# Performance work log

Hardware: AMD Instinct MI355X
Metric: run time of the kernel (lower is better)

Reference implementation:

```python
import jax, jax.numpy as jnp
import numpy as np

NUM_HEADS = 16
EPS = 1e-6


def setup_inputs() -> dict:
    key = jax.random.key(0)
    k1, k2, k3 = jax.random.split(key, 3)
    B, S, D = 4, 4096, 1024
    x = jax.random.normal(k1, (B, S, D), dtype=jnp.float32)
    # weights scaled like nn.Linear init (~1/sqrt(fan_in))
    Wqkv = jax.random.normal(k2, (D, 3 * D), dtype=jnp.float32) / np.sqrt(D)
    Wo = jax.random.normal(k3, (D, D), dtype=jnp.float32) / np.sqrt(D)
    return {"x": x, "Wqkv": Wqkv, "Wo": Wo}


def reference(x, Wqkv, Wo):
    B, S, D = x.shape
    H = NUM_HEADS
    hd = D // H
    qkv = x @ Wqkv                                   # [B,S,3D]
    qkv = qkv.reshape(B, S, 3, H, hd).transpose(2, 0, 3, 1, 4)
    Q, K, V = qkv[0], qkv[1], qkv[2]                 # [B,H,S,hd]
    # feature map: elu(x) + 1 (positive)
    Q = jax.nn.elu(Q) + 1.0
    K = jax.nn.elu(K) + 1.0
    # O(N d^2): KV state then Q contraction
    KV = jnp.einsum('bhnd,bhnv->bhdv', K, V)         # [B,H,hd,hd]
    out = jnp.einsum('bhnd,bhdv->bhnv', Q, KV)       # [B,H,S,hd]
    K_sum = K.sum(axis=2)                            # [B,H,hd]
    normalizer = jnp.einsum('bhnd,bhd->bhn', Q, K_sum)[..., None]  # [B,H,S,1]
    out = out / (normalizer + EPS)
    out = out.transpose(0, 2, 1, 3).reshape(B, S, D)
    return out @ Wo
```

## Files before the change

### kernel.cpp

```cpp
#include <hip/hip_runtime.h>

using u16 = unsigned short;
typedef __attribute__((ext_vector_type(8))) short short8;
typedef __attribute__((ext_vector_type(4))) float f32x4;

__device__ __forceinline__ u16 f2bf(float f) {
  unsigned int u = __float_as_uint(f);
  u = (u + 0x7FFFu + ((u >> 16) & 1u)) >> 16;
  return (u16)u;
}
__device__ __forceinline__ float bf2f(u16 v) {
  return __uint_as_float(((unsigned int)v) << 16);
}

__device__ __forceinline__ void gload16(const void* g, void* l) {
  __builtin_amdgcn_global_load_lds((const __attribute__((address_space(1))) void*)g,
                                   (__attribute__((address_space(3))) void*)l, 16, 0, 0);
}

#define B_ 4
#define S_ 4096
#define D_ 1024
#define H_ 16
#define HD_ 64
#define M_ (B_*S_)
#define N1_ (3*D_)
#define NSPLIT_ 4

#define OFF_XB    0ull
#define OFF_WQKVT (OFF_XB    + (size_t)M_*D_*2)
#define OFF_WOT   (OFF_WQKVT + (size_t)N1_*D_*2)
#define OFF_QBUF  (OFF_WOT   + (size_t)D_*D_*2)
#define OFF_KT    (OFF_QBUF  + (size_t)M_*D_*2)
#define OFF_VT    (OFF_KT    + (size_t)M_*D_*2)
#define OFF_KV    (OFF_VT    + (size_t)M_*D_*2)
#define OFF_KSUM  (OFF_KV    + (size_t)NSPLIT_*64*4096*4)
#define WS_NEEDED (OFF_KSUM  + (size_t)NSPLIT_*64*64*4)
#define OFF_WT    OFF_KT
#define OFF_KSG   (OFF_KT + (size_t)8*1024*1024)

__global__ __launch_bounds__(256) void prep_kernel(const float* __restrict__ x, u16* __restrict__ xb,
                                                   const float* __restrict__ Wqkv, u16* __restrict__ wqkvt,
                                                   const float* __restrict__ Wo, u16* __restrict__ wot)
{
  __shared__ float tile[32][33];
  int bid = blockIdx.x, tid = threadIdx.x;
  if (bid < 16384) {
    int i = bid * 256 + tid;
    float4 v = ((const float4*)x)[i];
    uint2 o;
    o.x = (unsigned)f2bf(v.x) | ((unsigned)f2bf(v.y) << 16);
    o.y = (unsigned)f2bf(v.z) | ((unsigned)f2bf(v.w) << 16);
    ((uint2*)xb)[i] = o;
    return;
  }
  const float* in; u16* out; int R, C, cb, rb;
  if (bid < 19456) {
    int t = bid - 16384;  in = Wqkv; out = wqkvt; R = D_; C = N1_;
    cb = t % 96; rb = t / 96;
  } else {
    int t = bid - 19456;  in = Wo; out = wot; R = D_; C = D_;
    cb = t % 32; rb = t / 32;
  }
  int tx = tid & 31, ty = tid >> 5;
  int c0 = cb * 32, r0 = rb * 32;
#pragma unroll
  for (int i = 0; i < 4; i++)
    tile[ty + i*8][tx] = in[(size_t)(r0 + ty + i*8) * C + c0 + tx];
  __syncthreads();
#pragma unroll
  for (int i = 0; i < 4; i++)
    out[(size_t)(c0 + ty + i*8) * R + r0 + tx] = f2bf(tile[tx][ty + i*8]);
}

template<int MODE>
__global__ __launch_bounds__(512, 2) void gemm256(
    const u16* __restrict__ A, const u16* __restrict__ Bt,
    float* __restrict__ Cf, u16* __restrict__ qout,
    u16* __restrict__ Kt, u16* __restrict__ Vt,
    int M, int N, int K)
{
  __shared__ __align__(16) char smem[131072];
  int tid = threadIdx.x;
  int w = tid >> 6, lane = tid & 63;
  int quad = lane >> 4, l16 = lane & 15;
  int wm = w >> 2, wn = w & 3;

  int nwg = gridDim.x * gridDim.y;
  int flat = blockIdx.y * gridDim.x + blockIdx.x;
  int wg = (flat & 7) * (nwg >> 3) + (flat >> 3);
  int bx = wg % gridDim.x, by = wg / gridDim.x;
  int bm = by * 256, bn = bx * 256;

  const u16* Bp;
  if constexpr (MODE == 2) Bp = Bt + ((size_t)(bm >> 12) << 20);
  else                     Bp = Bt;

  int prl = lane >> 3;
  int c4  = (lane & 7) ^ prl;
  int r0  = ((w << 3) + prl) * 2 + (c4 >> 2);
  int koff = (c4 & 3) * 8;
  const u16* gA0 = A  + (size_t)(bm + r0) * K + koff;
  const u16* gB0 = Bp + (size_t)(bn + r0) * K + koff;
  size_t rowskip = (size_t)128 * K;
  char* smemc = smem;
  int ldsAw = w * 1024;
  int ldsBw = 65536 + w * 1024;

  int ph = (((l16 & 1) << 2) | quad) ^ ((l16 >> 1) & 7);
  int baseA = wm * 8192 + (l16 >> 1) * 128 + ph * 16;
  int baseB = 65536 + wn * 4096 + (l16 >> 1) * 128 + ph * 16;

  f32x4 acc[8][4];
#pragma unroll
  for (int i = 0; i < 8; i++)
#pragma unroll
    for (int j = 0; j < 4; j++) acc[i][j] = (f32x4)0.0f;

  int nt = K >> 5;

#define STG(tt, slot) {                                                   \
    const u16* a0_ = gA0 + (tt) * 32;                                     \
    const u16* b0_ = gB0 + (tt) * 32;                                     \
    gload16(a0_,           smemc + (slot)*16384 + ldsAw);                 \
    gload16(a0_ + rowskip, smemc + (slot)*16384 + 8192 + ldsAw);          \
    gload16(b0_,           smemc + (slot)*16384 + ldsBw);                 \
    gload16(b0_ + rowskip, smemc + (slot)*16384 + 8192 + ldsBw);          \
  }

#define COMPUTE(slot) {                                                              \
    const char* sb = smemc + (slot) * 16384;                                         \
    short8 bfr[4], af[8];                                                            \
    _Pragma("unroll")                                                                \
    for (int nj = 0; nj < 4; nj++) bfr[nj] = *(const short8*)(sb + baseB + nj*1024); \
    _Pragma("unroll")                                                                \
    for (int mi = 0; mi < 8; mi++) af[mi] = *(const short8*)(sb + baseA + mi*1024);  \
    __builtin_amdgcn_s_setprio(1);                                                   \
    _Pragma("unroll")                                                                \
    for (int mi = 0; mi < 8; mi++)                                                   \
      _Pragma("unroll")                                                              \
      for (int nj = 0; nj < 4; nj++)                                                 \
        acc[mi][nj] = __builtin_amdgcn_mfma_f32_16x16x32_bf16(af[mi], bfr[nj],       \
                                                              acc[mi][nj], 0, 0, 0); \
    __builtin_amdgcn_s_setprio(0);                                                   \
  }

#define WAITBAR(n) {                                                      \
    asm volatile("s_waitcnt vmcnt(" #n ")" ::: "memory");                 \
    __builtin_amdgcn_s_barrier();                                         \
    asm volatile("" ::: "memory");                                        \
  }

  STG(0, 0); STG(1, 1); STG(2, 2);
  WAITBAR(8)

  for (int tb = 0; tb < nt - 4; tb += 4) {
#pragma unroll
    for (int i = 0; i < 4; ++i) {
      int t = tb + i;
      STG(t + 3, ((i + 3) & 3));
      COMPUTE(i)
      WAITBAR(8)
    }
  }

  STG(nt - 1, 3);
  COMPUTE(0)
  WAITBAR(8)
  COMPUTE(1)
  WAITBAR(4)
  COMPUTE(2)
  WAITBAR(0)
  COMPUTE(3)

#undef STG
#undef COMPUTE
#undef WAITBAR

  int colbase = bn + wn * 64;
  if constexpr (MODE != 1) {
#pragma unroll
    for (int mi = 0; mi < 8; mi++) {
      int row0 = bm + wm * 128 + mi * 16 + quad * 4;
#pragma unroll
      for (int nj = 0; nj < 4; nj++) {
        int col = colbase + nj * 16 + l16;
#pragma unroll
        for (int r = 0; r < 4; r++)
          Cf[(size_t)(row0 + r) * N + col] = acc[mi][nj][r];
      }
    }
  } else {
    int cls = colbase >> 10;
    if (cls == 0) {
#pragma unroll
      for (int mi = 0; mi < 8; mi++) {
        int row0 = bm + wm * 128 + mi * 16 + quad * 4;
#pragma unroll
        for (int nj = 0; nj < 4; nj++) {
          int col = colbase + nj * 16 + l16;
#pragma unroll
          for (int r = 0; r < 4; r++) {
            float v = acc[mi][nj][r];
            v = (v > 0.0f) ? (v + 1.0f) : __expf(v);
            qout[(size_t)(row0 + r) * D_ + col] = f2bf(v);
          }
        }
      }
    } else {
      int b = bm >> 12;
      int h = (colbase & 1023) >> 6;
      u16* dst = (cls == 1 ? Kt : Vt) + (size_t)((b * 16 + h) * 64) * 4096;
      int sb0 = (bm & 4095) + wm * 128;
      bool doElu = (cls == 1);
#pragma unroll
      for (int mi = 0; mi < 8; mi++) {
        int s = sb0 + mi * 16 + quad * 4;
#pragma unroll
        for (int nj = 0; nj < 4; nj++) {
          int d = nj * 16 + l16;
          float v0 = acc[mi][nj][0], v1 = acc[mi][nj][1], v2 = acc[mi][nj][2], v3 = acc[mi][nj][3];
          if (doElu) {
            v0 = (v0 > 0.0f) ? (v0 + 1.0f) : __expf(v0);
            v1 = (v1 > 0.0f) ? (v1 + 1.0f) : __expf(v1);
            v2 = (v2 > 0.0f) ? (v2 + 1.0f) : __expf(v2);
            v3 = (v3 > 0.0f) ? (v3 + 1.0f) : __expf(v3);
          }
          uint2 o;
          o.x = (unsigned)f2bf(v0) | ((unsigned)f2bf(v1) << 16);
          o.y = (unsigned)f2bf(v2) | ((unsigned)f2bf(v3) << 16);
          *(uint2*)(dst + (size_t)d * 4096 + s) = o;
        }
      }
    }
  }
}

__global__ __launch_bounds__(256) void kv_kernel(const u16* __restrict__ Kt,
                                                 const u16* __restrict__ Vt,
                                                 float* __restrict__ KVp,
                                                 float* __restrict__ Ksp)
{
  __shared__ float red[4096];
  __shared__ float redS[64];
  int tid = threadIdx.x;
  int bh = blockIdx.x;
  int ssplit = blockIdx.y;
  int wave = tid >> 6, lane = tid & 63, quad = lane >> 4, l16 = lane & 15;
  int sbase = ssplit * (S_ / NSPLIT_) + wave * (S_ / NSPLIT_ / 4);
  const u16* Kb = Kt + (size_t)bh * 64 * 4096;
  const u16* Vb = Vt + (size_t)bh * 64 * 4096;
  short8 ones;
#pragma unroll
  for (int e = 0; e < 8; ++e) ones[e] = (short)0x3F80;

  for (int i = tid; i < 4096; i += 256) red[i] = 0.0f;
  if (tid < 64) redS[tid] = 0.0f;

  f32x4 acc[4][4], accs[4];
#pragma unroll
  for (int i = 0; i < 4; i++) {
    accs[i] = (f32x4)0.0f;
#pragma unroll
    for (int j = 0; j < 4; j++) acc[i][j] = (f32x4)0.0f;
  }

  for (int kk = 0; kk < S_ / NSPLIT_ / 4 / 32; ++kk) {
    int s = sbase + kk * 32 + quad * 8;
    short8 af[4], bfr[4];
#pragma unroll
    for (int i = 0; i < 4; i++) {
      af[i]  = *(const short8*)(Kb + (size_t)(i*16 + l16) * 4096 + s);
      bfr[i] = *(const short8*)(Vb + (size_t)(i*16 + l16) * 4096 + s);
    }
#pragma unroll
    for (int i = 0; i < 4; i++) {
#pragma unroll
      for (int j = 0; j < 4; j++)
        acc[i][j] = __builtin_amdgcn_mfma_f32_16x16x32_bf16(af[i], bfr[j], acc[i][j], 0, 0, 0);
      accs[i] = __builtin_amdgcn_mfma_f32_16x16x32_bf16(af[i], ones, accs[i], 0, 0, 0);
    }
  }
  __syncthreads();
#pragma unroll
  for (int i = 0; i < 4; i++) {
    int d0 = i*16 + quad*4;
#pragma unroll
    for (int j = 0; j < 4; j++)
#pragma unroll
      for (int r = 0; r < 4; r++)
        atomicAdd(&red[(d0 + r) * 64 + j*16 + l16], acc[i][j][r]);
    if (l16 == 0)
#pragma unroll
      for (int r = 0; r < 4; r++)
        atomicAdd(&redS[d0 + r], accs[i][r]);
  }
  __syncthreads();
  float* dst = KVp + ((size_t)ssplit * 64 + bh) * 4096;
  for (int i = tid; i < 4096; i += 256) dst[i] = red[i];
  if (tid < 64) Ksp[((size_t)ssplit * 64 + bh) * 64 + tid] = redS[tid];
}

__global__ __launch_bounds__(256) void kvw_kernel(const float* __restrict__ KVp,
                                                  const float* __restrict__ Ksp,
                                                  const u16* __restrict__ wot,
                                                  u16* __restrict__ wt,
                                                  float* __restrict__ ksum)
{
  __shared__ u16 kvlds[4096];
  int tid = threadIdx.x;
  int ct = blockIdx.x;
  int bh = blockIdx.y;
  int b = bh >> 4, h = bh & 15;
  const float* kvsrc = KVp + (size_t)bh * 4096;
  for (int i = tid; i < 4096; i += 256) {
    float s = kvsrc[i] + kvsrc[i + 64*4096] + kvsrc[i + 2*64*4096] + kvsrc[i + 3*64*4096];
    kvlds[i] = f2bf(s);
  }
  if (ct == 0 && tid < 64) {
    const float* ks = Ksp + (size_t)bh * 64;
    ksum[bh * 64 + tid] = ks[tid] + ks[tid + 64*64] + ks[tid + 2*64*64] + ks[tid + 3*64*64];
  }
  __syncthreads();
  int w = tid >> 6, lane = tid & 63, quad = lane >> 4, l16 = lane & 15;

  short8 bfr[2][4];
#pragma unroll
  for (int ks = 0; ks < 2; ++ks)
#pragma unroll
    for (int nj = 0; nj < 4; ++nj)
      bfr[ks][nj] = *(const short8*)(&kvlds[(nj*16 + l16) * 64 + ks*32 + quad*8]);

  f32x4 acc[2][4];
#pragma unroll
  for (int i = 0; i < 2; i++)
#pragma unroll
    for (int j = 0; j < 4; j++) acc[i][j] = (f32x4)0.0f;

  int c0 = ct * 128 + w * 32;
#pragma unroll
  for (int ks = 0; ks < 2; ++ks) {
#pragma unroll
    for (int mi = 0; mi < 2; ++mi) {
      short8 af = *(const short8*)(wot + (size_t)(c0 + mi*16 + l16) * 1024 + h*64 + ks*32 + quad*8);
#pragma unroll
      for (int nj = 0; nj < 4; ++nj)
        acc[mi][nj] = __builtin_amdgcn_mfma_f32_16x16x32_bf16(af, bfr[ks][nj], acc[mi][nj], 0, 0, 0);
    }
  }
  u16* dst = wt + ((size_t)b << 20);
#pragma unroll
  for (int mi = 0; mi < 2; ++mi) {
    int c = c0 + mi*16 + quad*4;
#pragma unroll
    for (int nj = 0; nj < 4; ++nj) {
      int hd = h*64 + nj*16 + l16;
#pragma unroll
      for (int r = 0; r < 4; ++r)
        dst[(size_t)(c + r) * 1024 + hd] = f2bf(acc[mi][nj][r]);
    }
  }
}

__global__ __launch_bounds__(256) void qscale_kernel(u16* __restrict__ qbuf,
                                                     const float* __restrict__ ksum)
{
  __shared__ float ks[1024];
  int tid = threadIdx.x;
  int blk = blockIdx.x;
  int b = blk >> 10;
  for (int i = tid; i < 1024; i += 256) ks[i] = ksum[b * 1024 + i];
  __syncthreads();
  int wv = tid >> 6, ln = tid & 63;
  int s = blk * 4 + wv;
  u16* row = qbuf + (size_t)s * 1024 + ln * 16;
  short8 qa = *(const short8*)row;
  short8 qb = *(const short8*)(row + 8);
  int h4 = (ln >> 2) * 64 + (ln & 3) * 16;
  float p = 0.0f;
#pragma unroll
  for (int j = 0; j < 8; ++j) p += bf2f((u16)qa[j]) * ks[h4 + j];
#pragma unroll
  for (int j = 0; j < 8; ++j) p += bf2f((u16)qb[j]) * ks[h4 + 8 + j];
  p += __shfl_xor(p, 1);
  p += __shfl_xor(p, 2);
  float inv = 1.0f / (p + 1e-6f);
  short8 oa, ob;
#pragma unroll
  for (int j = 0; j < 8; ++j) {
    oa[j] = (short)f2bf(bf2f((u16)qa[j]) * inv);
    ob[j] = (short)f2bf(bf2f((u16)qb[j]) * inv);
  }
  *(short8*)row = oa;
  *(short8*)(row + 8) = ob;
}

extern "C" void kernel_launch(void* const* d_in, const int* in_sizes, int n_in,
                              void* d_out, int out_size, void* d_ws, size_t ws_size,
                              hipStream_t stream) {
  const float* x    = (const float*)d_in[0];
  const float* Wqkv = (const float*)d_in[1];
  const float* Wo   = (const float*)d_in[2];
  float* out = (float*)d_out;
  char* ws = (char*)d_ws;
  if (ws_size < WS_NEEDED) return;

  u16*   xb    = (u16*)  (ws + OFF_XB);
  u16*   wqkvt = (u16*)  (ws + OFF_WQKVT);
  u16*   wot   = (u16*)  (ws + OFF_WOT);
  u16*   qbuf  = (u16*)  (ws + OFF_QBUF);
  u16*   kt    = (u16*)  (ws + OFF_KT);
  u16*   vt    = (u16*)  (ws + OFF_VT);
  float* kvp   = (float*)(ws + OFF_KV);
  float* ksp   = (float*)(ws + OFF_KSUM);
  u16*   wt    = (u16*)  (ws + OFF_WT);
  float* ksg   = (float*)(ws + OFF_KSG);

  prep_kernel<<<20480, 256, 0, stream>>>(x, xb, Wqkv, wqkvt, Wo, wot);
  gemm256<1><<<dim3(N1_/256, M_/256), 512, 0, stream>>>(xb, wqkvt, nullptr, qbuf, kt, vt,
                                                        M_, N1_, D_);
  kv_kernel<<<dim3(64, NSPLIT_), 256, 0, stream>>>(kt, vt, kvp, ksp);
  kvw_kernel<<<dim3(8, 64), 256, 0, stream>>>(kvp, ksp, wot, wt, ksg);
  qscale_kernel<<<4096, 256, 0, stream>>>(qbuf, ksg);
  gemm256<2><<<dim3(D_/256, M_/256), 512, 0, stream>>>(qbuf, wt, out, nullptr, nullptr, nullptr,
                                                       M_, D_, D_);
}
```

Measured before the change: 337.8 us.

## Fuse K/V projection with per-tile KV outer-product reduction in GEMM epilogue

Splits the QKV projection into a Q-only GEMM and a K/V GEMM whose tiles pair matching K and V head columns. The K/V tile's epilogue stages the elu-transformed K and V in shared memory and computes partial K^T·V and K-sum per 256-row block with MFMA. This removes the global round trip of transposed K/V buffers and the separate kv_kernel. A new kvsum kernel reduces the 16 partials per batch-head. The cost is an extra epilogue in the GEMM, more partial-sum traffic, and two GEMM launches instead of one.

```diff
diff --git a/kernel.cpp b/kernel.cpp
--- a/kernel.cpp
+++ b/kernel.cpp
@@ -25,7 +25,6 @@
 #define HD_ 64
 #define M_ (B_*S_)
 #define N1_ (3*D_)
-#define NSPLIT_ 4
 
 #define OFF_XB    0ull
 #define OFF_WQKVT (OFF_XB    + (size_t)M_*D_*2)
@@ -34,10 +33,13 @@
 #define OFF_KT    (OFF_QBUF  + (size_t)M_*D_*2)
 #define OFF_VT    (OFF_KT    + (size_t)M_*D_*2)
 #define OFF_KV    (OFF_VT    + (size_t)M_*D_*2)
-#define OFF_KSUM  (OFF_KV    + (size_t)NSPLIT_*64*4096*4)
-#define WS_NEEDED (OFF_KSUM  + (size_t)NSPLIT_*64*64*4)
+#define OFF_KSUM  (OFF_KV    + (size_t)4*64*4096*4)
+#define WS_NEEDED (OFF_KSUM  + (size_t)4*64*64*4)
 #define OFF_WT    OFF_KT
-#define OFF_KSG   (OFF_KT + (size_t)8*1024*1024)
+#define OFF_KVS   (OFF_KT + ((size_t)8<<20))
+#define OFF_KSG   (OFF_KT + ((size_t)9<<20))
+#define OFF_KVPP  OFF_VT
+#define OFF_KSPP  (OFF_VT + ((size_t)16<<20))
 
 __global__ __launch_bounds__(256) void prep_kernel(const float* __restrict__ x, u16* __restrict__ xb,
                                                    const float* __restrict__ Wqkv, u16* __restrict__ wqkvt,
@@ -77,7 +79,7 @@
 __global__ __launch_bounds__(512, 2) void gemm256(
     const u16* __restrict__ A, const u16* __restrict__ Bt,
     float* __restrict__ Cf, u16* __restrict__ qout,
-    u16* __restrict__ Kt, u16* __restrict__ Vt,
+    float* __restrict__ P1, float* __restrict__ P2,
     int M, int N, int K)
 {
   __shared__ __align__(16) char smem[131072];
@@ -92,17 +94,24 @@
   int bx = wg % gridDim.x, by = wg / gridDim.x;
   int bm = by * 256, bn = bx * 256;
 
-  const u16* Bp;
-  if constexpr (MODE == 2) Bp = Bt + ((size_t)(bm >> 12) << 20);
-  else                     Bp = Bt;
-
   int prl = lane >> 3;
   int c4  = (lane & 7) ^ prl;
   int r0  = ((w << 3) + prl) * 2 + (c4 >> 2);
   int koff = (c4 & 3) * 8;
-  const u16* gA0 = A  + (size_t)(bm + r0) * K + koff;
-  const u16* gB0 = Bp + (size_t)(bn + r0) * K + koff;
-  size_t rowskip = (size_t)128 * K;
+  const u16* gA0 = A + (size_t)(bm + r0) * K + koff;
+  const u16* gB0;
+  size_t rowskipA = (size_t)128 * K;
+  size_t rowskipB;
+  if constexpr (MODE == 3) {
+    gB0 = Bt + (size_t)(1024 + bx * 128 + r0) * K + koff;
+    rowskipB = (size_t)1024 * K;
+  } else if constexpr (MODE == 2) {
+    gB0 = Bt + ((size_t)(bm >> 12) << 20) + (size_t)(bn + r0) * K + koff;
+    rowskipB = (size_t)128 * K;
+  } else {
+    gB0 = Bt + (size_t)(bn + r0) * K + koff;
+    rowskipB = (size_t)128 * K;
+  }
   char* smemc = smem;
   int ldsAw = w * 1024;
   int ldsBw = 65536 + w * 1024;
@@ -122,10 +131,10 @@
 #define STG(tt, slot) {                                                   \
     const u16* a0_ = gA0 + (tt) * 32;                                     \
     const u16* b0_ = gB0 + (tt) * 32;                                     \
-    gload16(a0_,           smemc + (slot)*16384 + ldsAw);                 \
-    gload16(a0_ + rowskip, smemc + (slot)*16384 + 8192 + ldsAw);          \
-    gload16(b0_,           smemc + (slot)*16384 + ldsBw);                 \
-    gload16(b0_ + rowskip, smemc + (slot)*16384 + 8192 + ldsBw);          \
+    gload16(a0_,            smemc + (slot)*16384 + ldsAw);                \
+    gload16(a0_ + rowskipA, smemc + (slot)*16384 + 8192 + ldsAw);         \
+    gload16(b0_,            smemc + (slot)*16384 + ldsBw);                \
+    gload16(b0_ + rowskipB, smemc + (slot)*16384 + 8192 + ldsBw);         \
   }
 
 #define COMPUTE(slot) {                                                              \
@@ -177,8 +186,8 @@
 #undef COMPUTE
 #undef WAITBAR
 
-  int colbase = bn + wn * 64;
-  if constexpr (MODE != 1) {
+  if constexpr (MODE == 2) {
+    int colbase = bn + wn * 64;
 #pragma unroll
     for (int mi = 0; mi < 8; mi++) {
       int row0 = bm + wm * 128 + mi * 16 + quad * 4;
@@ -190,35 +199,36 @@
           Cf[(size_t)(row0 + r) * N + col] = acc[mi][nj][r];
       }
     }
-  } else {
-    int cls = colbase >> 10;
-    if (cls == 0) {
-#pragma unroll
-      for (int mi = 0; mi < 8; mi++) {
-        int row0 = bm + wm * 128 + mi * 16 + quad * 4;
-#pragma unroll
-        for (int nj = 0; nj < 4; nj++) {
-          int col = colbase + nj * 16 + l16;
-#pragma unroll
-          for (int r = 0; r < 4; r++) {
-            float v = acc[mi][nj][r];
-            v = (v > 0.0f) ? (v + 1.0f) : __expf(v);
-            qout[(size_t)(row0 + r) * D_ + col] = f2bf(v);
-          }
+  } else if constexpr (MODE == 1) {
+#pragma unroll
+    for (int mi = 0; mi < 8; mi++) {
+      int row0 = bm + wm * 128 + mi * 16 + quad * 4;
+#pragma unroll
+      for (int nj = 0; nj < 4; nj++) {
+        int col = bn + wn * 64 + nj * 16 + l16;
+#pragma unroll
+        for (int r = 0; r < 4; r++) {
+          float v = acc[mi][nj][r];
+          v = (v > 0.0f) ? (v + 1.0f) : __expf(v);
+          qout[(size_t)(row0 + r) * D_ + col] = f2bf(v);
         }
       }
-    } else {
-      int b = bm >> 12;
-      int h = (colbase & 1023) >> 6;
-      u16* dst = (cls == 1 ? Kt : Vt) + (size_t)((b * 16 + h) * 64) * 4096;
-      int sb0 = (bm & 4095) + wm * 128;
-      bool doElu = (cls == 1);
+    }
+  } else {
+    __syncthreads();
+    {
+      char* basekv = smemc + ((wn < 2) ? 0 : 65536);
+      bool doElu = (wn < 2);
 #pragma unroll
       for (int mi = 0; mi < 8; mi++) {
-        int s = sb0 + mi * 16 + quad * 4;
+        int sb = wm * 128 + mi * 16 + quad * 4;
+        int slot = sb >> 5;
+        int kc = (sb >> 3) & 3;
+        int so = (sb & 7) * 2;
 #pragma unroll
         for (int nj = 0; nj < 4; nj++) {
-          int d = nj * 16 + l16;
+          int dv = (wn & 1) * 64 + nj * 16 + l16;
+          int pc = (((dv & 1) << 2) | kc) ^ ((dv >> 1) & 7);
           float v0 = acc[mi][nj][0], v1 = acc[mi][nj][1], v2 = acc[mi][nj][2], v3 = acc[mi][nj][3];
           if (doElu) {
             v0 = (v0 > 0.0f) ? (v0 + 1.0f) : __expf(v0);
@@ -229,98 +239,99 @@
           uint2 o;
           o.x = (unsigned)f2bf(v0) | ((unsigned)f2bf(v1) << 16);
           o.y = (unsigned)f2bf(v2) | ((unsigned)f2bf(v3) << 16);
-          *(uint2*)(dst + (size_t)d * 4096 + s) = o;
+          *(uint2*)(basekv + slot*8192 + (dv >> 1)*128 + pc*16 + so) = o;
         }
       }
     }
-  }
-}
-
-__global__ __launch_bounds__(256) void kv_kernel(const u16* __restrict__ Kt,
-                                                 const u16* __restrict__ Vt,
-                                                 float* __restrict__ KVp,
-                                                 float* __restrict__ Ksp)
+    __syncthreads();
+    int hh = w >> 2, dh = w & 1, vh = (w >> 1) & 1;
+    short8 ones;
+#pragma unroll
+    for (int e = 0; e < 8; ++e) ones[e] = (short)0x3F80;
+    f32x4 a2[2][2], s2[2];
+#pragma unroll
+    for (int i = 0; i < 2; i++) {
+      s2[i] = (f32x4)0.0f;
+#pragma unroll
+      for (int j = 0; j < 2; j++) a2[i][j] = (f32x4)0.0f;
+    }
+#pragma unroll
+    for (int t = 0; t < 8; t++) {
+      short8 ak[2], bv[2];
+#pragma unroll
+      for (int i = 0; i < 2; i++) {
+        int d = hh * 64 + dh * 32 + i * 16 + l16;
+        ak[i] = *(const short8*)(smemc + t*8192 + (d >> 1)*128 +
+                                 (((((d & 1) << 2) | quad)) ^ ((d >> 1) & 7))*16);
+        int v = hh * 64 + vh * 32 + i * 16 + l16;
+        bv[i] = *(const short8*)(smemc + 65536 + t*8192 + (v >> 1)*128 +
+                                 (((((v & 1) << 2) | quad)) ^ ((v >> 1) & 7))*16);
+      }
+#pragma unroll
+      for (int i = 0; i < 2; i++) {
+#pragma unroll
+        for (int j = 0; j < 2; j++)
+          a2[i][j] = __builtin_amdgcn_mfma_f32_16x16x32_bf16(ak[i], bv[j], a2[i][j], 0, 0, 0);
+        if (vh == 0)
+          s2[i] = __builtin_amdgcn_mfma_f32_16x16x32_bf16(ak[i], ones, s2[i], 0, 0, 0);
+      }
+    }
+    int p = bx;
+    int mb = bm >> 8;
+    float* kdst = P1 + (size_t)(mb * 16 + p * 2 + hh) * 4096;
+#pragma unroll
+    for (int i = 0; i < 2; i++)
+#pragma unroll
+      for (int j = 0; j < 2; j++)
+#pragma unroll
+        for (int r = 0; r < 4; r++)
+          kdst[(dh*32 + i*16 + quad*4 + r) * 64 + vh*32 + j*16 + l16] = a2[i][j][r];
+    if (vh == 0 && l16 == 0) {
+      float* sdst = P2 + (size_t)(mb * 16 + p * 2 + hh) * 64;
+#pragma unroll
+      for (int i = 0; i < 2; i++)
+#pragma unroll
+        for (int r = 0; r < 4; r++)
+          sdst[dh*32 + i*16 + quad*4 + r] = s2[i][r];
+    }
+  }
+}
+
+__global__ __launch_bounds__(256) void kvsum_kernel(const float* __restrict__ kvpp,
+                                                    const float* __restrict__ kspp,
+                                                    float* __restrict__ kvp,
+                                                    float* __restrict__ ksg)
 {
-  __shared__ float red[4096];
-  __shared__ float redS[64];
-  int tid = threadIdx.x;
-  int bh = blockIdx.x;
-  int ssplit = blockIdx.y;
-  int wave = tid >> 6, lane = tid & 63, quad = lane >> 4, l16 = lane & 15;
-  int sbase = ssplit * (S_ / NSPLIT_) + wave * (S_ / NSPLIT_ / 4);
-  const u16* Kb = Kt + (size_t)bh * 64 * 4096;
-  const u16* Vb = Vt + (size_t)bh * 64 * 4096;
-  short8 ones;
-#pragma unroll
-  for (int e = 0; e < 8; ++e) ones[e] = (short)0x3F80;
-
-  for (int i = tid; i < 4096; i += 256) red[i] = 0.0f;
-  if (tid < 64) redS[tid] = 0.0f;
-
-  f32x4 acc[4][4], accs[4];
-#pragma unroll
-  for (int i = 0; i < 4; i++) {
-    accs[i] = (f32x4)0.0f;
-#pragma unroll
-    for (int j = 0; j < 4; j++) acc[i][j] = (f32x4)0.0f;
-  }
-
-  for (int kk = 0; kk < S_ / NSPLIT_ / 4 / 32; ++kk) {
-    int s = sbase + kk * 32 + quad * 8;
-    short8 af[4], bfr[4];
-#pragma unroll
-    for (int i = 0; i < 4; i++) {
-      af[i]  = *(const short8*)(Kb + (size_t)(i*16 + l16) * 4096 + s);
-      bfr[i] = *(const short8*)(Vb + (size_t)(i*16 + l16) * 4096 + s);
-    }
-#pragma unroll
-    for (int i = 0; i < 4; i++) {
-#pragma unroll
-      for (int j = 0; j < 4; j++)
-        acc[i][j] = __builtin_amdgcn_mfma_f32_16x16x32_bf16(af[i], bfr[j], acc[i][j], 0, 0, 0);
-      accs[i] = __builtin_amdgcn_mfma_f32_16x16x32_bf16(af[i], ones, accs[i], 0, 0, 0);
-    }
-  }
-  __syncthreads();
-#pragma unroll
-  for (int i = 0; i < 4; i++) {
-    int d0 = i*16 + quad*4;
-#pragma unroll
-    for (int j = 0; j < 4; j++)
-#pragma unroll
-      for (int r = 0; r < 4; r++)
-        atomicAdd(&red[(d0 + r) * 64 + j*16 + l16], acc[i][j][r]);
-    if (l16 == 0)
-#pragma unroll
-      for (int r = 0; r < 4; r++)
-        atomicAdd(&redS[d0 + r], accs[i][r]);
-  }
-  __syncthreads();
-  float* dst = KVp + ((size_t)ssplit * 64 + bh) * 4096;
-  for (int i = tid; i < 4096; i += 256) dst[i] = red[i];
-  if (tid < 64) Ksp[((size_t)ssplit * 64 + bh) * 64 + tid] = redS[tid];
-}
-
-__global__ __launch_bounds__(256) void kvw_kernel(const float* __restrict__ KVp,
-                                                  const float* __restrict__ Ksp,
+  int tid = threadIdx.x, bh = blockIdx.x;
+  int b = bh >> 4, phh = bh & 15;
+  int base = b * 256 + phh;
+  for (int i = tid; i < 4096; i += 256) {
+    float s = 0.0f;
+#pragma unroll
+    for (int m = 0; m < 16; ++m)
+      s += kvpp[(size_t)(base + m * 16) * 4096 + i];
+    kvp[(size_t)bh * 4096 + i] = s;
+  }
+  if (tid < 64) {
+    float s = 0.0f;
+#pragma unroll
+    for (int m = 0; m < 16; ++m)
+      s += kspp[(size_t)(base + m * 16) * 64 + tid];
+    ksg[bh * 64 + tid] = s;
+  }
+}
+
+__global__ __launch_bounds__(256) void kvw_kernel(const float* __restrict__ kvp,
                                                   const u16* __restrict__ wot,
-                                                  u16* __restrict__ wt,
-                                                  float* __restrict__ ksum)
+                                                  u16* __restrict__ wt)
 {
   __shared__ u16 kvlds[4096];
   int tid = threadIdx.x;
   int ct = blockIdx.x;
   int bh = blockIdx.y;
   int b = bh >> 4, h = bh & 15;
-  const float* kvsrc = KVp + (size_t)bh * 4096;
-  for (int i = tid; i < 4096; i += 256) {
-    float s = kvsrc[i] + kvsrc[i + 64*4096] + kvsrc[i + 2*64*4096] + kvsrc[i + 3*64*4096];
-    kvlds[i] = f2bf(s);
-  }
-  if (ct == 0 && tid < 64) {
-    const float* ks = Ksp + (size_t)bh * 64;
-    ksum[bh * 64 + tid] = ks[tid] + ks[tid + 64*64] + ks[tid + 2*64*64] + ks[tid + 3*64*64];
-  }
+  const float* kvsrc = kvp + (size_t)bh * 4096;
+  for (int i = tid; i < 4096; i += 256) kvlds[i] = f2bf(kvsrc[i]);
   __syncthreads();
   int w = tid >> 6, lane = tid & 63, quad = lane >> 4, l16 = lane & 15;
 
@@ -409,19 +420,20 @@
   u16*   wqkvt = (u16*)  (ws + OFF_WQKVT);
   u16*   wot   = (u16*)  (ws + OFF_WOT);
   u16*   qbuf  = (u16*)  (ws + OFF_QBUF);
-  u16*   kt    = (u16*)  (ws + OFF_KT);
-  u16*   vt    = (u16*)  (ws + OFF_VT);
-  float* kvp   = (float*)(ws + OFF_KV);
-  float* ksp   = (float*)(ws + OFF_KSUM);
   u16*   wt    = (u16*)  (ws + OFF_WT);
+  float* kvs   = (float*)(ws + OFF_KVS);
   float* ksg   = (float*)(ws + OFF_KSG);
+  float* kvpp  = (float*)(ws + OFF_KVPP);
+  float* kspp  = (float*)(ws + OFF_KSPP);
 
   prep_kernel<<<20480, 256, 0, stream>>>(x, xb, Wqkv, wqkvt, Wo, wot);
-  gemm256<1><<<dim3(N1_/256, M_/256), 512, 0, stream>>>(xb, wqkvt, nullptr, qbuf, kt, vt,
-                                                        M_, N1_, D_);
-  kv_kernel<<<dim3(64, NSPLIT_), 256, 0, stream>>>(kt, vt, kvp, ksp);
-  kvw_kernel<<<dim3(8, 64), 256, 0, stream>>>(kvp, ksp, wot, wt, ksg);
+  gemm256<3><<<dim3(8, M_/256), 512, 0, stream>>>(xb, wqkvt, nullptr, nullptr, kvpp, kspp,
+                                                  M_, N1_, D_);
+  gemm256<1><<<dim3(4, M_/256), 512, 0, stream>>>(xb, wqkvt, nullptr, qbuf, nullptr, nullptr,
+                                                  M_, N1_, D_);
+  kvsum_kernel<<<64, 256, 0, stream>>>(kvpp, kspp, kvs, ksg);
+  kvw_kernel<<<dim3(8, 64), 256, 0, stream>>>(kvs, wot, wt);
   qscale_kernel<<<4096, 256, 0, stream>>>(qbuf, ksg);
-  gemm256<2><<<dim3(D_/256, M_/256), 512, 0, stream>>>(qbuf, wt, out, nullptr, nullptr, nullptr,
-                                                       M_, D_, D_);
-}
+  gemm256<2><<<dim3(4, M_/256), 512, 0, stream>>>(qbuf, wt, out, nullptr, nullptr, nullptr,
+                                                  M_, D_, D_);
+}
```

Result: faster. 293.2 us (-13.2%).
